# Optimization experiments

Hardware: AMD Instinct MI355X
Metric: run time of the kernel (lower is better)

## Reference

```python
import jax, jax.numpy as jnp
import numpy as np

B, S, HID, H, D, F = 8, 256, 1024, 16, 64, 64
BASE_LR = 0.1
MAX_STEPS = 4
EPS = 1e-5


def _ln(x, g, b):
    mu = jnp.mean(x, axis=-1, keepdims=True)
    var = jnp.var(x, axis=-1, keepdims=True)
    return (x - mu) * jax.lax.rsqrt(var + EPS) * g + b


def setup_inputs() -> dict:
    key = jax.random.key(0)
    ks = jax.random.split(key, 10)
    n = lambda i, shape, s=0.02: jax.random.normal(ks[i], shape, jnp.float32) * s
    return {
        "x": jax.random.normal(ks[0], (B, S, HID), jnp.float32),
        "wq": n(1, (HID, HID)),
        "wk": n(2, (HID, HID)),
        "wv": n(3, (HID, HID)),
        "fw_w1": n(4, (H, D, F), 0.05),
        "fw_b1": jnp.zeros((H, F), jnp.float32),
        "fw_w2": n(5, (H, F, D), 0.05),
        "fw_b2": jnp.zeros((H, D), jnp.float32),
        "fw_ln_g": jnp.ones((H, D), jnp.float32),
        "fw_ln_b": jnp.zeros((H, D), jnp.float32),
        "loss_w": n(6, (D, D)),
        "loss_b": jnp.zeros((D,), jnp.float32),
        "ttt_g": jnp.ones((H, D), jnp.float32),
        "ttt_b": jnp.zeros((H, D), jnp.float32),
        "wo": n(7, (HID, HID)),
        "wg": n(8, (HID, HID)),
        "pn_g": jnp.ones((HID,), jnp.float32),
        "pn_b": jnp.zeros((HID,), jnp.float32),
    }


def _fw_apply(p, kx):
    # per-head fast-weight MLP: kx (B,H,D) -> (B,H,D)
    w1, b1, w2, b2, lg, lb = p
    h = jax.nn.gelu(jnp.einsum('bhd,hdf->bhf', kx, w1) + b1)
    o = jnp.einsum('bhf,hfd->bhd', h, w2) + b2
    return _ln(o, lg, lb)


def _forward(x, wq, wk, wv, fw_w1, fw_b1, fw_w2, fw_b2, fw_ln_g, fw_ln_b,
             loss_w, loss_b, ttt_g, ttt_b, wo, wg, pn_g, pn_b):
    # projections (torch Linear with W stored as (in,out) here: y = x @ W)
    q = (x @ wq).reshape(B, S, H, D)
    k = (x @ wk).reshape(B, S, H, D)
    v = (x @ wv).reshape(B, S, H, D)
    # scan over tokens: xs shaped (S, B, H, D)
    qs = jnp.swapaxes(q, 0, 1)
    ks_ = jnp.swapaxes(k, 0, 1)
    vs = jnp.swapaxes(v, 0, 1)

    def token_step(p, qkv):
        q_t, k_t, v_t = qkv  # (B,H,D) each
        target = v_t - k_t

        def loss_fn(pp):
            z = _fw_apply(pp, k_t)
            pred = jnp.einsum('bhd,de->bhe', z, loss_w) + loss_b
            return jnp.mean((pred - target) ** 2)

        for _ in range(MAX_STEPS):
            g = jax.grad(loss_fn)(p)
            p = jax.tree.map(lambda a, gg: a - BASE_LR * gg, p, g)
        z = _fw_apply(p, k_t)
        z = _ln(z, ttt_g, ttt_b)  # per-head post-TTT LayerNorm
        return p, q_t + z

    p0 = (fw_w1, fw_b1, fw_w2, fw_b2, fw_ln_g, fw_ln_b)
    _, outs = jax.lax.scan(token_step, p0, (qs, ks_, vs))
    out = jnp.swapaxes(outs, 0, 1).reshape(B, S, HID)
    gated = jax.nn.gelu(x @ wg) * _ln(out, pn_g, pn_b)
    return gated @ wo


def reference(x, wq, wk, wv, fw_w1, fw_b1, fw_w2, fw_b2, fw_ln_g, fw_ln_b,
              loss_w, loss_b, ttt_g, ttt_b, wo, wg, pn_g, pn_b):
    return _forward(x, wq, wk, wv, fw_w1, fw_b1, fw_w2, fw_b2, fw_ln_g, fw_ln_b,
                    loss_w, loss_b, ttt_g, ttt_b, wo, wg, pn_g, pn_b)
```

## Files before the change

### kernel.cpp

```cpp
#include <hip/hip_runtime.h>

#define Bv 8
#define Sv 256
#define Hv 16
#define Dv 64
#define LR 0.1f
#define SCALE (2.0f / 8192.0f)

using bf16x8 = __attribute__((ext_vector_type(8))) short;
using bf16x4 = __attribute__((ext_vector_type(4))) short;
using f32x4  = __attribute__((ext_vector_type(4))) float;
using u32x4  = __attribute__((ext_vector_type(4))) unsigned;
#define MFMA16(A, B, C) __builtin_amdgcn_mfma_f32_16x16x32_bf16(A, B, C, 0, 0, 0)

constexpr int U_W1T = 0;
constexpr int U_W2T = 8704;
constexpr int U_W2R = 17408;
constexpr int U_G   = 26112;
constexpr int U_LwR = 34816;
constexpr int U_K   = 43520;
constexpr int U_H   = 45696;
constexpr int U_Z   = 47872;
constexpr int U_TG  = 50048;
constexpr int U_DO  = 52224;
constexpr int U_KT  = 54400;
constexpr int U_HT  = 55424;
constexpr int U_DOT = 56448;
constexpr int U_DAT = 57472;
constexpr int F_BASE = 29248;
constexpr int F_O   = F_BASE;
constexpr int F_XH  = F_BASE + 544;
constexpr int F_GD  = F_XH + 544;
constexpr int F_TGL = F_GD + 544;
constexpr int F_B1  = F_TGL + 544;
constexpr int F_B2  = F_B1 + 64;
constexpr int F_LG  = F_B2 + 64;
constexpr int F_LB  = F_LG + 64;
constexpr int F_C1  = F_LB + 64;
constexpr int F_TGm = F_C1 + 64;
constexpr int F_TBm = F_TGm + 64;
constexpr int F_RSTD = F_TBm + 64;
constexpr int U_KG  = (F_RSTD + 8) * 2;
constexpr int U_HT2 = U_KG + 256;
constexpr int LDS_BYTES = (U_HT2 + 1024) * 2;

__device__ __forceinline__ short bf_rn(float v) {
    unsigned u = __float_as_uint(v);
    unsigned r = u + 0x7fffu + ((u >> 16) & 1u);
    return (short)(r >> 16);
}
__device__ __forceinline__ void cvt1(float v, short &hi, short &lo) {
    hi = bf_rn(v);
    float hf = __uint_as_float(((unsigned)(unsigned short)hi) << 16);
    lo = bf_rn(v - hf);
}
__device__ __forceinline__ float bf2f(short u) {
    return __uint_as_float(((unsigned)(unsigned short)u) << 16);
}
__device__ __forceinline__ unsigned cvtpk(float a, float b) {
    unsigned r;
    asm("v_cvt_pk_bf16_f32 %0, %1, %2" : "=v"(r) : "v"(a), "v"(b));
    return r;
}
__device__ __forceinline__ void cvt2(float a, float b, unsigned &hw,
                                     unsigned &lw) {
    hw = cvtpk(a, b);
    float ra = a - __uint_as_float(hw << 16);
    float rb = b - __uint_as_float(hw & 0xffff0000u);
    lw = cvtpk(ra, rb);
}
template <int CTRL>
__device__ __forceinline__ float dpp_add(float v) {
    int s = __builtin_amdgcn_update_dpp(0, __float_as_int(v), CTRL, 0xF, 0xF,
                                        true);
    return v + __int_as_float(s);
}
__device__ __forceinline__ float red32(float v) {
    v = dpp_add<0xB1>(v);
    v = dpp_add<0x4E>(v);
    v = dpp_add<0x124>(v);
    v = dpp_add<0x128>(v);
    v += __shfl_xor(v, 16);
    return v;
}
__device__ __forceinline__ float fast_tanh(float u) {
    u = fminf(fmaxf(u, -10.f), 10.f);
    float e = __expf(2.0f * u);
    return (e - 1.0f) / (e + 1.0f);
}
__device__ __forceinline__ void gelu_both(float x, float &g, float &dg) {
    const float C0 = 0.7978845608028654f, A0 = 0.044715f;
    float x2 = x * x;
    float u = C0 * x * (1.0f + A0 * x2);
    float t = fast_tanh(u);
    g = 0.5f * x * (1.0f + t);
    float du = C0 * (1.0f + 3.0f * A0 * x2);
    dg = 0.5f * (1.0f + t) + 0.5f * x * (1.0f - t * t) * du;
}
__device__ __forceinline__ float gelu_f(float x) {
    const float C0 = 0.7978845608028654f, A0 = 0.044715f;
    float u = C0 * x * (1.0f + A0 * x * x);
    return 0.5f * x * (1.0f + fast_tanh(u));
}

__device__ __forceinline__ f32x4 mm64(const unsigned short *Ap,
                                      const unsigned short *Bp,
                                      int w, int c, int q) {
    const unsigned short *ar = Ap + c * 136 + 8 * q;
    const unsigned short *br = Bp + (16 * w + c) * 136 + 8 * q;
    bf16x8 ah0 = *(const bf16x8 *)(ar);
    bf16x8 al0 = *(const bf16x8 *)(ar + 64);
    bf16x8 bh0 = *(const bf16x8 *)(br);
    bf16x8 bl0 = *(const bf16x8 *)(br + 64);
    bf16x8 ah1 = *(const bf16x8 *)(ar + 32);
    bf16x8 al1 = *(const bf16x8 *)(ar + 96);
    bf16x8 bh1 = *(const bf16x8 *)(br + 32);
    bf16x8 bl1 = *(const bf16x8 *)(br + 96);
    f32x4 x0 = {0.f, 0.f, 0.f, 0.f}, x1 = {0.f, 0.f, 0.f, 0.f};
    x0 = MFMA16(ah0, bh0, x0); x1 = MFMA16(ah1, bh1, x1);
    x0 = MFMA16(al0, bh0, x0); x1 = MFMA16(al1, bh1, x1);
    x0 = MFMA16(ah0, bl0, x0); x1 = MFMA16(ah1, bl1, x1);
    return x0 + x1;
}

__device__ __forceinline__ void updW3(const bf16x8 *a4, bf16x8 b,
                                      float (&m)[16], unsigned short *WT,
                                      int w, int c, int q) {
    f32x4 g[4];
#pragma unroll
    for (int mt = 0; mt < 4; ++mt) {
        f32x4 z = {0.f, 0.f, 0.f, 0.f};
        g[mt] = MFMA16(a4[mt], b, z);
    }
    unsigned short *p0 = &WT[(16 * w + c) * 136 + 4 * q];
#pragma unroll
    for (int mt = 0; mt < 4; ++mt) {
        m[mt * 4 + 0] -= LR * g[mt][0];
        m[mt * 4 + 1] -= LR * g[mt][1];
        m[mt * 4 + 2] -= LR * g[mt][2];
        m[mt * 4 + 3] -= LR * g[mt][3];
        unsigned nh0, nl0, nh1, nl1;
        cvt2(m[mt * 4 + 0], m[mt * 4 + 1], nh0, nl0);
        cvt2(m[mt * 4 + 2], m[mt * 4 + 3], nh1, nl1);
        uint2 nh, nl;
        nh.x = nh0; nh.y = nh1;
        nl.x = nl0; nl.y = nl1;
        *(uint2 *)(p0 + 16 * mt) = nh;
        *(uint2 *)(p0 + 16 * mt + 64) = nl;
    }
}

__global__ __launch_bounds__(256) void ttt_scan(
    const float *__restrict__ q_g, const float *__restrict__ k_g,
    const float *__restrict__ v_g, float *__restrict__ out_g,
    const float *__restrict__ fw_w1, const float *__restrict__ fw_b1,
    const float *__restrict__ fw_w2, const float *__restrict__ fw_b2,
    const float *__restrict__ fw_lng, const float *__restrict__ fw_lnb,
    const float *__restrict__ loss_w, const float *__restrict__ loss_bv,
    const float *__restrict__ ttt_gv, const float *__restrict__ ttt_bv) {
    extern __shared__ char smem[];
    unsigned short *us = (unsigned short *)smem;
    float *fs = (float *)smem;

    unsigned short *W1T = us + U_W1T, *W2T = us + U_W2T, *W2R = us + U_W2R;
    unsigned short *Gp = us + U_G, *LwR = us + U_LwR;
    unsigned short *Kp = us + U_K, *Hp = us + U_H, *Zp = us + U_Z;
    unsigned short *TGp = us + U_TG, *DOp = us + U_DO;
    unsigned short *KT = us + U_KT, *HT0 = us + U_HT;
    unsigned short *DOT = us + U_DOT;
    unsigned short *KgT = us + U_KG, *HT1 = us + U_HT2;
    float *o_s = fs + F_O, *xh_s = fs + F_XH;
    float *b2_s = fs + F_B2, *lg_s = fs + F_LG;
    float *lb_s = fs + F_LB, *c1_s = fs + F_C1;
    float *tG_s = fs + F_TGm, *tB_s = fs + F_TBm, *rstd_s = fs + F_RSTD;

    const int h = blockIdx.x, tid = threadIdx.x;
    const int w = tid >> 6, lane = tid & 63, c = lane & 15, q = lane >> 4;
    const int bb = tid >> 5, j0 = (tid & 31) * 2;

    for (int i = tid; i < 4096; i += 256) {
        int r = i >> 6, cc = i & 63;
        short hi, lo;
        cvt1(fw_w1[h * 4096 + i], hi, lo);
        W1T[cc * 136 + r] = (unsigned short)hi;
        W1T[cc * 136 + 64 + r] = (unsigned short)lo;
        cvt1(fw_w2[h * 4096 + i], hi, lo);
        W2T[cc * 136 + r] = (unsigned short)hi;
        W2T[cc * 136 + 64 + r] = (unsigned short)lo;
        W2R[r * 136 + cc] = (unsigned short)hi;
        W2R[r * 136 + 64 + cc] = (unsigned short)lo;
        cvt1(loss_w[i], hi, lo);
        LwR[r * 136 + cc] = (unsigned short)hi;
        LwR[r * 136 + 64 + cc] = (unsigned short)lo;
    }
    for (int i = tid; i < 5 * 8 * 128; i += 256) {
        int a = i / 128, u = i % 128;
        int arr = a >> 3, row = 8 + (a & 7);
        unsigned short *base = (arr == 0) ? Kp : (arr == 1) ? Hp
                              : (arr == 2) ? Zp : (arr == 3) ? TGp : DOp;
        base[row * 136 + u] = 0;
    }
    float w1m[16], w2m[16], w2rm[16];
#pragma unroll
    for (int mt = 0; mt < 4; ++mt) {
#pragma unroll
        for (int r = 0; r < 4; ++r) {
            int el = 16 * mt + 4 * q + r;
            int row = 16 * w + c;
            w1m[mt * 4 + r] = fw_w1[h * 4096 + el * 64 + row];
            w2m[mt * 4 + r] = fw_w2[h * 4096 + el * 64 + row];
            w2rm[mt * 4 + r] = fw_w2[h * 4096 + row * 64 + el];
        }
    }
    __syncthreads();
#pragma unroll 1
    for (int mt = 0; mt < 4; ++mt) {
        f32x4 g = mm64(LwR + 16 * 136 * mt, LwR, w, c, q);
#pragma unroll
        for (int r = 0; r < 4; ++r) {
            short hi, lo;
            cvt1(g[r], hi, lo);
            int dr = 16 * mt + 4 * q + r, dc = 16 * w + c;
            Gp[dr * 136 + dc] = (unsigned short)hi;
            Gp[dr * 136 + 64 + dc] = (unsigned short)lo;
        }
    }
    if (tid < 64) {
        b2_s[tid] = fw_b2[h * 64 + tid];
        lg_s[tid] = fw_lng[h * 64 + tid];
        lb_s[tid] = fw_lnb[h * 64 + tid];
        tG_s[tid] = ttt_gv[h * 64 + tid];
        tB_s[tid] = ttt_bv[h * 64 + tid];
        float c1 = 0.f;
        for (int e = 0; e < 64; ++e) c1 += loss_bv[e] * loss_w[tid * 64 + e];
        c1_s[tid] = c1;
    }

    float2 pk, pv, pq, q_cur;
    {
        int idx = ((bb * Sv + 0) * Hv + h) * Dv + j0;
        float2 k0 = *(const float2 *)&k_g[idx];
        float2 v0 = *(const float2 *)&v_g[idx];
        q_cur = *(const float2 *)&q_g[idx];
        unsigned khw, klw;
        cvt2(k0.x, k0.y, khw, klw);
        *(unsigned *)&Kp[bb * 136 + j0] = khw;
        *(unsigned *)&Kp[bb * 136 + 64 + j0] = klw;
        KT[j0 * 16 + bb] = (unsigned short)khw;
        KT[j0 * 16 + 8 + bb] = (unsigned short)klw;
        KT[(j0 + 1) * 16 + bb] = (unsigned short)(khw >> 16);
        KT[(j0 + 1) * 16 + 8 + bb] = (unsigned short)(klw >> 16);
        unsigned thw, tlw;
        cvt2(v0.x - k0.x, v0.y - k0.y, thw, tlw);
        *(unsigned *)&TGp[bb * 136 + j0] = thw;
        *(unsigned *)&TGp[bb * 136 + 64 + j0] = tlw;
    }
    float b1_r = (q < 2) ? fw_b1[h * 64 + 16 * w + c] : 0.f;
    __syncthreads();
    float c1_r = c1_s[16 * w + c];
    f32x4 gd_r = {0.f, 0.f, 0.f, 0.f};
    f32x4 tgl_r = {0.f, 0.f, 0.f, 0.f};

#pragma unroll 1
    for (int t = 0; t < Sv; ++t) {
        if (t + 1 < Sv) {
            int idx2 = ((bb * Sv + t + 1) * Hv + h) * Dv + j0;
            pk = *(const float2 *)&k_g[idx2];
            pv = *(const float2 *)&v_g[idx2];
            pq = *(const float2 *)&q_g[idx2];
        }

        f32x4 acc1 = mm64(Kp, W1T, w, c, q);
        {
            f32x4 a2 = mm64(TGp, LwR, w, c, q);
            if (q < 2) {
#pragma unroll
                for (int r = 0; r < 4; ++r) tgl_r[r] = a2[r] - c1_r;
            }
        }
        if (w == 0) {
            f32x4 kg = mm64(Kp, Kp, 0, c, q);
            if (q < 2) {
#pragma unroll
                for (int r = 0; r < 4; ++r) {
                    short hi, lo;
                    cvt1(-LR * kg[r], hi, lo);
                    KgT[c * 16 + 4 * q + r] = (unsigned short)hi;
                    KgT[c * 16 + 8 + 4 * q + r] = (unsigned short)lo;
                }
            }
        }
        if (q < 2) {
            int col = 16 * w + c;
            float gv[4];
#pragma unroll
            for (int r = 0; r < 4; ++r) {
                float g, dg;
                gelu_both(acc1[r] + b1_r, g, dg);
                gv[r] = g;
                gd_r[r] = dg;
            }
            unsigned h01, l01, h23, l23;
            cvt2(gv[0], gv[1], h01, l01);
            cvt2(gv[2], gv[3], h23, l23);
            Hp[(4 * q + 0) * 136 + col] = (unsigned short)h01;
            Hp[(4 * q + 1) * 136 + col] = (unsigned short)(h01 >> 16);
            Hp[(4 * q + 2) * 136 + col] = (unsigned short)h23;
            Hp[(4 * q + 3) * 136 + col] = (unsigned short)(h23 >> 16);
            Hp[(4 * q + 0) * 136 + 64 + col] = (unsigned short)l01;
            Hp[(4 * q + 1) * 136 + 64 + col] = (unsigned short)(l01 >> 16);
            Hp[(4 * q + 2) * 136 + 64 + col] = (unsigned short)l23;
            Hp[(4 * q + 3) * 136 + 64 + col] = (unsigned short)(l23 >> 16);
            uint2 hh, hl;
            hh.x = h01; hh.y = h23;
            hl.x = l01; hl.y = l23;
            *(uint2 *)&HT0[col * 16 + 4 * q] = hh;
            *(uint2 *)&HT0[col * 16 + 8 + 4 * q] = hl;
        }
        __syncthreads();

#pragma unroll 1
        for (int step = 0; step < 4; ++step) {
            const unsigned short *HTr = (step & 1) ? HT1 : HT0;
            unsigned short *HTw = (step & 1) ? HT0 : HT1;
            f32x4 acc = mm64(Hp, W2T, w, c, q);
            if (q < 2) {
                float bias = b2_s[16 * w + c];
#pragma unroll
                for (int r = 0; r < 4; ++r)
                    o_s[(4 * q + r) * 68 + 16 * w + c] = acc[r] + bias;
            }
            __syncthreads();
            float xh0_r, xh1_r;
            {
                float2 xv = *(const float2 *)&o_s[bb * 68 + j0];
                float s = red32(xv.x + xv.y);
                float s2 = red32(xv.x * xv.x + xv.y * xv.y);
                float mu = s * (1.f / 64.f);
                float var = s2 * (1.f / 64.f) - mu * mu;
                float rs = rsqrtf(var + 1e-5f);
                float xh0 = (xv.x - mu) * rs, xh1 = (xv.y - mu) * rs;
                float2 xw; xw.x = xh0; xw.y = xh1;
                *(float2 *)&xh_s[bb * 68 + j0] = xw;
                float z0 = xh0 * lg_s[j0] + lb_s[j0];
                float z1 = xh1 * lg_s[j0 + 1] + lb_s[j0 + 1];
                unsigned zh, zl;
                cvt2(z0, z1, zh, zl);
                *(unsigned *)&Zp[bb * 136 + j0] = zh;
                *(unsigned *)&Zp[bb * 136 + 64 + j0] = zl;
                if ((tid & 31) == 0) rstd_s[bb] = rs;
                xh0_r = xh0; xh1_r = xh1;
            }
            __syncthreads();
            acc = mm64(Zp, Gp, w, c, q);
            if (q < 2) {
                int col = 16 * w + c;
#pragma unroll
                for (int r = 0; r < 4; ++r)
                    o_s[(4 * q + r) * 68 + col] = (acc[r] - tgl_r[r]) * SCALE;
            }
            __syncthreads();
            {
                float2 dzv = *(const float2 *)&o_s[bb * 68 + j0];
                float dxh0 = dzv.x * lg_s[j0], dxh1 = dzv.y * lg_s[j0 + 1];
                float S1 = red32(dxh0 + dxh1) * (1.f / 64.f);
                float S2 = red32(dxh0 * xh0_r + dxh1 * xh1_r) * (1.f / 64.f);
                float rs = rstd_s[bb];
                float do0 = rs * (dxh0 - S1 - xh0_r * S2);
                float do1 = rs * (dxh1 - S1 - xh1_r * S2);
                unsigned dh, dl;
                cvt2(do0, do1, dh, dl);
                *(unsigned *)&DOp[bb * 136 + j0] = dh;
                *(unsigned *)&DOp[bb * 136 + 64 + j0] = dl;
                DOT[j0 * 16 + bb] = (unsigned short)dh;
                DOT[j0 * 16 + 8 + bb] = (unsigned short)dl;
                DOT[(j0 + 1) * 16 + bb] = (unsigned short)(dh >> 16);
                DOT[(j0 + 1) * 16 + 8 + bb] = (unsigned short)(dl >> 16);
            }
            __syncthreads();
            bf16x8 zf8;
#pragma unroll
            for (int j = 0; j < 8; ++j) zf8[j] = 0;
            bf16x8 aK[4], aH[4], aD[4];
#pragma unroll
            for (int mt = 0; mt < 4; ++mt) {
                aK[mt] = *(const bf16x8 *)&KT[(16 * mt + c) * 16 + (q & 1) * 8];
                aH[mt] = *(const bf16x8 *)&HTr[(16 * mt + c) * 16 + (q & 1) * 8];
                aD[mt] = *(const bf16x8 *)&DOT[(16 * mt + c) * 16 + (q & 1) * 8];
            }
            bf16x8 bDO = zf8, bHT = zf8;
            if (q < 2) {
                bDO = *(const bf16x8 *)&DOT[(16 * w + c) * 16];
                bHT = *(const bf16x8 *)&HTr[(16 * w + c) * 16];
            } else if (q == 2) {
                bDO = *(const bf16x8 *)&DOT[(16 * w + c) * 16 + 8];
                bHT = *(const bf16x8 *)&HTr[(16 * w + c) * 16 + 8];
            }
            bf16x8 aKg = *(const bf16x8 *)&KgT[c * 16 + (q & 1) * 8];
            acc = mm64(DOp, W2R, w, c, q);
            {
                float b1sum = 0.f;
                uint2 th; th.x = 0u; th.y = 0u;
                uint2 tl; tl.x = 0u; tl.y = 0u;
                if (q < 2) {
                    float da0 = acc[0] * gd_r[0];
                    float da1 = acc[1] * gd_r[1];
                    float da2 = acc[2] * gd_r[2];
                    float da3 = acc[3] * gd_r[3];
                    b1sum = da0 + da1 + da2 + da3;
                    unsigned h01, l01, h23, l23;
                    cvt2(da0, da1, h01, l01);
                    cvt2(da2, da3, h23, l23);
                    th.x = h01; th.y = h23;
                    tl.x = l01; tl.y = l23;
                }
                b1sum += __shfl_xor(b1sum, 16);
                unsigned hx0 = (unsigned)__shfl((int)th.x, c);
                unsigned hy0 = (unsigned)__shfl((int)th.y, c);
                unsigned hx1 = (unsigned)__shfl((int)th.x, c + 16);
                unsigned hy1 = (unsigned)__shfl((int)th.y, c + 16);
                unsigned lx0 = (unsigned)__shfl((int)tl.x, c);
                unsigned ly0 = (unsigned)__shfl((int)tl.y, c);
                unsigned lx1 = (unsigned)__shfl((int)tl.x, c + 16);
                unsigned ly1 = (unsigned)__shfl((int)tl.y, c + 16);
                u32x4 Bw = {0u, 0u, 0u, 0u};
                if (q < 2) {
                    Bw[0] = hx0; Bw[1] = hy0; Bw[2] = hx1; Bw[3] = hy1;
                } else if (q == 2) {
                    Bw[0] = lx0; Bw[1] = ly0; Bw[2] = lx1; Bw[3] = ly1;
                }
                bf16x8 bDA = __builtin_bit_cast(bf16x8, Bw);
                updW3(aK, bDA, w1m, W1T, w, c, q);
                updW3(aH, bDO, w2m, W2T, w, c, q);
                updW3(aD, bHT, w2rm, W2R, w, c, q);
                if (w == 2) {
                    bf16x8 oh_ = *(const bf16x8 *)&DOT[lane * 16];
                    bf16x8 ol_ = *(const bf16x8 *)&DOT[lane * 16 + 8];
                    float db2 = 0.f;
#pragma unroll
                    for (int j = 0; j < 8; ++j)
                        db2 += bf2f(oh_[j]) + bf2f(ol_[j]);
                    b2_s[lane] -= LR * db2;
                } else if (w == 3) {
                    float dlb = 0.f, dlg = 0.f;
#pragma unroll
                    for (int b = 0; b < 8; ++b) {
                        float dzv = o_s[b * 68 + lane];
                        dlb += dzv;
                        dlg += dzv * xh_s[b * 68 + lane];
                    }
                    lb_s[lane] -= LR * dlb;
                    lg_s[lane] -= LR * dlg;
                }
                acc1 = MFMA16(aKg, bDA, acc1);
                b1_r -= LR * b1sum;
                if (q < 2) {
                    int col = 16 * w + c;
                    if (step < 3) {
                        float gv[4];
#pragma unroll
                        for (int r = 0; r < 4; ++r) {
                            float g, dg;
                            gelu_both(acc1[r] + b1_r, g, dg);
                            gv[r] = g;
                            gd_r[r] = dg;
                        }
                        unsigned h01, l01, h23, l23;
                        cvt2(gv[0], gv[1], h01, l01);
                        cvt2(gv[2], gv[3], h23, l23);
                        Hp[(4 * q + 0) * 136 + col] = (unsigned short)h01;
                        Hp[(4 * q + 1) * 136 + col] = (unsigned short)(h01 >> 16);
                        Hp[(4 * q + 2) * 136 + col] = (unsigned short)h23;
                        Hp[(4 * q + 3) * 136 + col] = (unsigned short)(h23 >> 16);
                        Hp[(4 * q + 0) * 136 + 64 + col] = (unsigned short)l01;
                        Hp[(4 * q + 1) * 136 + 64 + col] = (unsigned short)(l01 >> 16);
                        Hp[(4 * q + 2) * 136 + 64 + col] = (unsigned short)l23;
                        Hp[(4 * q + 3) * 136 + 64 + col] = (unsigned short)(l23 >> 16);
                        uint2 hh, hl;
                        hh.x = h01; hh.y = h23;
                        hl.x = l01; hl.y = l23;
                        *(uint2 *)&HTw[col * 16 + 4 * q] = hh;
                        *(uint2 *)&HTw[col * 16 + 8 + 4 * q] = hl;
                    } else {
                        float gv[4];
#pragma unroll
                        for (int r = 0; r < 4; ++r)
                            gv[r] = gelu_f(acc1[r] + b1_r);
                        unsigned h01, l01, h23, l23;
                        cvt2(gv[0], gv[1], h01, l01);
                        cvt2(gv[2], gv[3], h23, l23);
                        Hp[(4 * q + 0) * 136 + col] = (unsigned short)h01;
                        Hp[(4 * q + 1) * 136 + col] = (unsigned short)(h01 >> 16);
                        Hp[(4 * q + 2) * 136 + col] = (unsigned short)h23;
                        Hp[(4 * q + 3) * 136 + col] = (unsigned short)(h23 >> 16);
                        Hp[(4 * q + 0) * 136 + 64 + col] = (unsigned short)l01;
                        Hp[(4 * q + 1) * 136 + 64 + col] = (unsigned short)(l01 >> 16);
                        Hp[(4 * q + 2) * 136 + 64 + col] = (unsigned short)l23;
                        Hp[(4 * q + 3) * 136 + 64 + col] = (unsigned short)(l23 >> 16);
                    }
                }
            }
            __syncthreads();
        }

        f32x4 acc = mm64(Hp, W2T, w, c, q);
        if (q < 2) {
            float bias = b2_s[16 * w + c];
#pragma unroll
            for (int r = 0; r < 4; ++r)
                o_s[(4 * q + r) * 68 + 16 * w + c] = acc[r] + bias;
        }
        if (t + 1 < Sv) {
            unsigned khw, klw;
            cvt2(pk.x, pk.y, khw, klw);
            *(unsigned *)&Kp[bb * 136 + j0] = khw;
            *(unsigned *)&Kp[bb * 136 + 64 + j0] = klw;
            KT[j0 * 16 + bb] = (unsigned short)khw;
            KT[j0 * 16 + 8 + bb] = (unsigned short)klw;
            KT[(j0 + 1) * 16 + bb] = (unsigned short)(khw >> 16);
            KT[(j0 + 1) * 16 + 8 + bb] = (unsigned short)(klw >> 16);
            unsigned thw, tlw;
            cvt2(pv.x - pk.x, pv.y - pk.y, thw, tlw);
            *(unsigned *)&TGp[bb * 136 + j0] = thw;
            *(unsigned *)&TGp[bb * 136 + 64 + j0] = tlw;
        }
        __syncthreads();
        {
            float2 xv = *(const float2 *)&o_s[bb * 68 + j0];
            float s = red32(xv.x + xv.y);
            float s2 = red32(xv.x * xv.x + xv.y * xv.y);
            float mu = s * (1.f / 64.f);
            float var = s2 * (1.f / 64.f) - mu * mu;
            float rs = rsqrtf(var + 1e-5f);
            float z0 = (xv.x - mu) * rs * lg_s[j0] + lb_s[j0];
            float z1 = (xv.y - mu) * rs * lg_s[j0 + 1] + lb_s[j0 + 1];
            float sb = red32(z0 + z1);
            float s2b = red32(z0 * z0 + z1 * z1);
            float mu2 = sb * (1.f / 64.f);
            float var2 = s2b * (1.f / 64.f) - mu2 * mu2;
            float rs2 = rsqrtf(var2 + 1e-5f);
            float z20 = (z0 - mu2) * rs2 * tG_s[j0] + tB_s[j0];
            float z21 = (z1 - mu2) * rs2 * tG_s[j0 + 1] + tB_s[j0 + 1];
            int idx = ((bb * Sv + t) * Hv + h) * Dv + j0;
            float2 ov;
            ov.x = q_cur.x + z20;
            ov.y = q_cur.y + z21;
            *(float2 *)&out_g[idx] = ov;
            q_cur = pq;
        }
    }
}

__device__ __forceinline__ void gemm_body(
    const float *__restrict__ A, const float *__restrict__ B,
    float *__restrict__ C, const float *__restrict__ gate_ln,
    int N, int K, int mode, int bm, int bn,
    unsigned short *As, unsigned short *Bs, int tid) {
    const int w = tid >> 6, lane = tid & 63, c = lane & 15, q = lane >> 4;

    f32x4 acc[4] = {{0.f, 0.f, 0.f, 0.f}, {0.f, 0.f, 0.f, 0.f},
                    {0.f, 0.f, 0.f, 0.f}, {0.f, 0.f, 0.f, 0.f}};
    const int srow = tid >> 2, sseg = (tid & 3) * 16;
    const int nB = tid & 63, kb = (tid >> 6) * 16;

    for (int k0 = 0; k0 < K; k0 += 64) {
        {
            const float *src = A + (long)(bm + srow) * K + k0 + sseg;
#pragma unroll
            for (int j = 0; j < 16; j += 2) {
                float2 v = *(const float2 *)(src + j);
                unsigned hw, lw;
                cvt2(v.x, v.y, hw, lw);
                *(unsigned *)&As[srow * 136 + sseg + j] = hw;
                *(unsigned *)&As[srow * 136 + 64 + sseg + j] = lw;
            }
        }
        {
            const float *bsrc = B + (long)(k0 + kb) * N + bn + nB;
#pragma unroll
            for (int j = 0; j < 16; j += 2) {
                float f0 = bsrc[(long)j * N];
                float f1 = bsrc[(long)(j + 1) * N];
                unsigned hw, lw;
                cvt2(f0, f1, hw, lw);
                *(unsigned *)&Bs[nB * 136 + kb + j] = hw;
                *(unsigned *)&Bs[nB * 136 + 64 + kb + j] = lw;
            }
        }
        __syncthreads();
#pragma unroll
        for (int kc = 0; kc < 2; ++kc) {
            const unsigned short *br =
                &Bs[(16 * w + c) * 136 + kc * 32 + 8 * q];
            bf16x8 bh = *(const bf16x8 *)(br);
            bf16x8 bl = *(const bf16x8 *)(br + 64);
#pragma unroll
            for (int mt = 0; mt < 4; ++mt) {
                const unsigned short *ar =
                    &As[(16 * mt + c) * 136 + kc * 32 + 8 * q];
                bf16x8 ah = *(const bf16x8 *)(ar);
                bf16x8 al = *(const bf16x8 *)(ar + 64);
                acc[mt] = MFMA16(ah, bh, acc[mt]);
                acc[mt] = MFMA16(al, bh, acc[mt]);
                acc[mt] = MFMA16(ah, bl, acc[mt]);
            }
        }
        __syncthreads();
    }
#pragma unroll
    for (int mt = 0; mt < 4; ++mt) {
#pragma unroll
        for (int r = 0; r < 4; ++r) {
            int row = bm + 16 * mt + 4 * q + r;
            int col = bn + 16 * w + c;
            float val = acc[mt][r];
            if (mode == 1)
                val = gelu_f(val) * gate_ln[(long)row * N + col];
            C[(long)row * N + col] = val;
        }
    }
}

__global__ __launch_bounds__(256) void gemm_bf16(
    const float *__restrict__ A, const float *__restrict__ B,
    float *__restrict__ C, const float *__restrict__ gate_ln,
    int M, int N, int K, int mode) {
    __shared__ unsigned short As[64 * 136];
    __shared__ unsigned short Bs[64 * 136];
    gemm_body(A, B, C, gate_ln, N, K, mode, blockIdx.y * 64, blockIdx.x * 64,
              As, Bs, threadIdx.x);
}

__global__ __launch_bounds__(256) void gemm_qkv(
    const float *__restrict__ A, const float *__restrict__ Wq_,
    const float *__restrict__ Wk_, const float *__restrict__ Wv_,
    float *__restrict__ Cq, float *__restrict__ Ck, float *__restrict__ Cv_,
    int N, int K) {
    __shared__ unsigned short As[64 * 136];
    __shared__ unsigned short Bs[64 * 136];
    const int mat = blockIdx.x >> 4;
    const int bn = (blockIdx.x & 15) * 64;
    const float *Bmat = (mat == 0) ? Wq_ : (mat == 1) ? Wk_ : Wv_;
    float *Cmat = (mat == 0) ? Cq : (mat == 1) ? Ck : Cv_;
    gemm_body(A, Bmat, Cmat, nullptr, N, K, 0, blockIdx.y * 64, bn, As, Bs,
              threadIdx.x);
}

__global__ __launch_bounds__(256) void row_ln(const float *__restrict__ in,
                                              float *__restrict__ out,
                                              const float *__restrict__ g,
                                              const float *__restrict__ b) {
    __shared__ float sred[4], s2red[4];
    const int row = blockIdx.x;
    const int tid = threadIdx.x;
    const float *x = in + (long)row * 1024;
    float4 v = *(const float4 *)(x + tid * 4);
    float s = v.x + v.y + v.z + v.w;
    float s2 = v.x * v.x + v.y * v.y + v.z * v.z + v.w * v.w;
#pragma unroll
    for (int m = 1; m <= 32; m <<= 1) {
        s += __shfl_xor(s, m);
        s2 += __shfl_xor(s2, m);
    }
    if ((tid & 63) == 0) {
        sred[tid >> 6] = s;
        s2red[tid >> 6] = s2;
    }
    __syncthreads();
    float S = sred[0] + sred[1] + sred[2] + sred[3];
    float S2 = s2red[0] + s2red[1] + s2red[2] + s2red[3];
    float mu = S * (1.f / 1024.f);
    float var = S2 * (1.f / 1024.f) - mu * mu;
    float rs = rsqrtf(var + 1e-5f);
    float o[4] = {v.x, v.y, v.z, v.w};
    float4 ov;
    float r[4];
#pragma unroll
    for (int i = 0; i < 4; ++i) {
        int col = tid * 4 + i;
        r[i] = (o[i] - mu) * rs * g[col] + b[col];
    }
    ov.x = r[0]; ov.y = r[1]; ov.z = r[2]; ov.w = r[3];
    *(float4 *)(out + (long)row * 1024 + tid * 4) = ov;
}

extern "C" void kernel_launch(void *const *d_in, const int *in_sizes, int n_in,
                              void *d_out, int out_size, void *d_ws,
                              size_t ws_size, hipStream_t stream) {
    const float *x = (const float *)d_in[0];
    const float *wq = (const float *)d_in[1];
    const float *wk = (const float *)d_in[2];
    const float *wv = (const float *)d_in[3];
    const float *fw_w1 = (const float *)d_in[4];
    const float *fw_b1 = (const float *)d_in[5];
    const float *fw_w2 = (const float *)d_in[6];
    const float *fw_b2 = (const float *)d_in[7];
    const float *fw_lng = (const float *)d_in[8];
    const float *fw_lnb = (const float *)d_in[9];
    const float *loss_w = (const float *)d_in[10];
    const float *loss_b = (const float *)d_in[11];
    const float *ttt_g = (const float *)d_in[12];
    const float *ttt_b = (const float *)d_in[13];
    const float *wo = (const float *)d_in[14];
    const float *wg = (const float *)d_in[15];
    const float *pn_g = (const float *)d_in[16];
    const float *pn_b = (const float *)d_in[17];

    const long MAT = 2048L * 1024L;
    float *q_ws = (float *)d_ws;
    float *k_ws = q_ws + MAT;
    float *v_ws = k_ws + MAT;
    float *out_ws = v_ws + MAT;
    float *ln_ws = k_ws;
    float *gated_ws = v_ws;

    dim3 gq(16 * 3, 2048 / 64), gg(1024 / 64, 2048 / 64), bt(256);
    hipLaunchKernelGGL(gemm_qkv, gq, bt, 0, stream, x, wq, wk, wv,
                       q_ws, k_ws, v_ws, 1024, 1024);

    (void)hipFuncSetAttribute((const void *)ttt_scan,
                              hipFuncAttributeMaxDynamicSharedMemorySize,
                              LDS_BYTES);
    hipLaunchKernelGGL(ttt_scan, dim3(16), dim3(256), LDS_BYTES, stream,
                       q_ws, k_ws, v_ws, out_ws, fw_w1, fw_b1, fw_w2, fw_b2,
                       fw_lng, fw_lnb, loss_w, loss_b, ttt_g, ttt_b);

    hipLaunchKernelGGL(row_ln, dim3(2048), dim3(256), 0, stream, out_ws, ln_ws,
                       pn_g, pn_b);
    hipLaunchKernelGGL(gemm_bf16, gg, bt, 0, stream, x, wg, gated_ws, ln_ws,
                       2048, 1024, 1024, 1);
    hipLaunchKernelGGL(gemm_bf16, gg, bt, 0, stream, gated_ws, wo,
                       (float *)d_out, (const float *)nullptr, 2048, 1024,
                       1024, 0);
}
```

Before: 3.702 ms.

## Overlap gate GEMM with the TTT scan by running it in extra blocks

The x@wg gate GEMM with its GELU now runs in 512 extra blocks of the ttt_scan launch, so it executes on otherwise idle CUs while the 16 scan blocks work. Its result is written to the output buffer as scratch. A small elementwise kernel then multiplies it by the layer-normed TTT output, replacing the fused gate GEMM that used to run after the scan. The cost is an extra read and write of a 2048x1024 tensor, plus the extra blocks taking the large dynamic LDS allocation, which can limit how many fit per CU.

Result: no change. 3.700 ms (-0.0%).

```diff
diff --git a/kernel.cpp b/kernel.cpp
--- a/kernel.cpp
+++ b/kernel.cpp
@@ -150,6 +150,78 @@
     }
 }
 
+__device__ __forceinline__ void gemm_body(
+    const float *__restrict__ A, const float *__restrict__ B,
+    float *__restrict__ C, const float *__restrict__ gate_ln,
+    int N, int K, int mode, int bm, int bn,
+    unsigned short *As, unsigned short *Bs, int tid) {
+    const int w = tid >> 6, lane = tid & 63, c = lane & 15, q = lane >> 4;
+
+    f32x4 acc[4] = {{0.f, 0.f, 0.f, 0.f}, {0.f, 0.f, 0.f, 0.f},
+                    {0.f, 0.f, 0.f, 0.f}, {0.f, 0.f, 0.f, 0.f}};
+    const int srow = tid >> 2, sseg = (tid & 3) * 16;
+    const int nB = tid & 63, kb = (tid >> 6) * 16;
+
+    for (int k0 = 0; k0 < K; k0 += 64) {
+        {
+            const float *src = A + (long)(bm + srow) * K + k0 + sseg;
+#pragma unroll
+            for (int j = 0; j < 16; j += 2) {
+                float2 v = *(const float2 *)(src + j);
+                unsigned hw, lw;
+                cvt2(v.x, v.y, hw, lw);
+                *(unsigned *)&As[srow * 136 + sseg + j] = hw;
+                *(unsigned *)&As[srow * 136 + 64 + sseg + j] = lw;
+            }
+        }
+        {
+            const float *bsrc = B + (long)(k0 + kb) * N + bn + nB;
+#pragma unroll
+            for (int j = 0; j < 16; j += 2) {
+                float f0 = bsrc[(long)j * N];
+                float f1 = bsrc[(long)(j + 1) * N];
+                unsigned hw, lw;
+                cvt2(f0, f1, hw, lw);
+                *(unsigned *)&Bs[nB * 136 + kb + j] = hw;
+                *(unsigned *)&Bs[nB * 136 + 64 + kb + j] = lw;
+            }
+        }
+        __syncthreads();
+#pragma unroll
+        for (int kc = 0; kc < 2; ++kc) {
+            const unsigned short *br =
+                &Bs[(16 * w + c) * 136 + kc * 32 + 8 * q];
+            bf16x8 bh = *(const bf16x8 *)(br);
+            bf16x8 bl = *(const bf16x8 *)(br + 64);
+#pragma unroll
+            for (int mt = 0; mt < 4; ++mt) {
+                const unsigned short *ar =
+                    &As[(16 * mt + c) * 136 + kc * 32 + 8 * q];
+                bf16x8 ah = *(const bf16x8 *)(ar);
+                bf16x8 al = *(const bf16x8 *)(ar + 64);
+                acc[mt] = MFMA16(ah, bh, acc[mt]);
+                acc[mt] = MFMA16(al, bh, acc[mt]);
+                acc[mt] = MFMA16(ah, bl, acc[mt]);
+            }
+        }
+        __syncthreads();
+    }
+#pragma unroll
+    for (int mt = 0; mt < 4; ++mt) {
+#pragma unroll
+        for (int r = 0; r < 4; ++r) {
+            int row = bm + 16 * mt + 4 * q + r;
+            int col = bn + 16 * w + c;
+            float val = acc[mt][r];
+            if (mode == 1)
+                val = gelu_f(val) * gate_ln[(long)row * N + col];
+            else if (mode == 3)
+                val = gelu_f(val);
+            C[(long)row * N + col] = val;
+        }
+    }
+}
+
 __global__ __launch_bounds__(256) void ttt_scan(
     const float *__restrict__ q_g, const float *__restrict__ k_g,
     const float *__restrict__ v_g, float *__restrict__ out_g,
@@ -157,10 +229,20 @@
     const float *__restrict__ fw_w2, const float *__restrict__ fw_b2,
     const float *__restrict__ fw_lng, const float *__restrict__ fw_lnb,
     const float *__restrict__ loss_w, const float *__restrict__ loss_bv,
-    const float *__restrict__ ttt_gv, const float *__restrict__ ttt_bv) {
+    const float *__restrict__ ttt_gv, const float *__restrict__ ttt_bv,
+    const float *__restrict__ gx, const float *__restrict__ gwg,
+    float *__restrict__ ggo) {
     extern __shared__ char smem[];
     unsigned short *us = (unsigned short *)smem;
     float *fs = (float *)smem;
+    const int tid = threadIdx.x;
+
+    if (blockIdx.x >= Hv) {
+        int bid = blockIdx.x - Hv;
+        gemm_body(gx, gwg, ggo, nullptr, 1024, 1024, 3,
+                  (bid >> 4) * 64, (bid & 15) * 64, us, us + 64 * 136, tid);
+        return;
+    }
 
     unsigned short *W1T = us + U_W1T, *W2T = us + U_W2T, *W2R = us + U_W2R;
     unsigned short *Gp = us + U_G, *LwR = us + U_LwR;
@@ -174,7 +256,7 @@
     float *lb_s = fs + F_LB, *c1_s = fs + F_C1;
     float *tG_s = fs + F_TGm, *tB_s = fs + F_TBm, *rstd_s = fs + F_RSTD;
 
-    const int h = blockIdx.x, tid = threadIdx.x;
+    const int h = blockIdx.x;
     const int w = tid >> 6, lane = tid & 63, c = lane & 15, q = lane >> 4;
     const int bb = tid >> 5, j0 = (tid & 31) * 2;
 
@@ -551,76 +633,6 @@
     }
 }
 
-__device__ __forceinline__ void gemm_body(
-    const float *__restrict__ A, const float *__restrict__ B,
-    float *__restrict__ C, const float *__restrict__ gate_ln,
-    int N, int K, int mode, int bm, int bn,
-    unsigned short *As, unsigned short *Bs, int tid) {
-    const int w = tid >> 6, lane = tid & 63, c = lane & 15, q = lane >> 4;
-
-    f32x4 acc[4] = {{0.f, 0.f, 0.f, 0.f}, {0.f, 0.f, 0.f, 0.f},
-                    {0.f, 0.f, 0.f, 0.f}, {0.f, 0.f, 0.f, 0.f}};
-    const int srow = tid >> 2, sseg = (tid & 3) * 16;
-    const int nB = tid & 63, kb = (tid >> 6) * 16;
-
-    for (int k0 = 0; k0 < K; k0 += 64) {
-        {
-            const float *src = A + (long)(bm + srow) * K + k0 + sseg;
-#pragma unroll
-            for (int j = 0; j < 16; j += 2) {
-                float2 v = *(const float2 *)(src + j);
-                unsigned hw, lw;
-                cvt2(v.x, v.y, hw, lw);
-                *(unsigned *)&As[srow * 136 + sseg + j] = hw;
-                *(unsigned *)&As[srow * 136 + 64 + sseg + j] = lw;
-            }
-        }
-        {
-            const float *bsrc = B + (long)(k0 + kb) * N + bn + nB;
-#pragma unroll
-            for (int j = 0; j < 16; j += 2) {
-                float f0 = bsrc[(long)j * N];
-                float f1 = bsrc[(long)(j + 1) * N];
-                unsigned hw, lw;
-                cvt2(f0, f1, hw, lw);
-                *(unsigned *)&Bs[nB * 136 + kb + j] = hw;
-                *(unsigned *)&Bs[nB * 136 + 64 + kb + j] = lw;
-            }
-        }
-        __syncthreads();
-#pragma unroll
-        for (int kc = 0; kc < 2; ++kc) {
-            const unsigned short *br =
-                &Bs[(16 * w + c) * 136 + kc * 32 + 8 * q];
-            bf16x8 bh = *(const bf16x8 *)(br);
-            bf16x8 bl = *(const bf16x8 *)(br + 64);
-#pragma unroll
-            for (int mt = 0; mt < 4; ++mt) {
-                const unsigned short *ar =
-                    &As[(16 * mt + c) * 136 + kc * 32 + 8 * q];
-                bf16x8 ah = *(const bf16x8 *)(ar);
-                bf16x8 al = *(const bf16x8 *)(ar + 64);
-                acc[mt] = MFMA16(ah, bh, acc[mt]);
-                acc[mt] = MFMA16(al, bh, acc[mt]);
-                acc[mt] = MFMA16(ah, bl, acc[mt]);
-            }
-        }
-        __syncthreads();
-    }
-#pragma unroll
-    for (int mt = 0; mt < 4; ++mt) {
-#pragma unroll
-        for (int r = 0; r < 4; ++r) {
-            int row = bm + 16 * mt + 4 * q + r;
-            int col = bn + 16 * w + c;
-            float val = acc[mt][r];
-            if (mode == 1)
-                val = gelu_f(val) * gate_ln[(long)row * N + col];
-            C[(long)row * N + col] = val;
-        }
-    }
-}
-
 __global__ __launch_bounds__(256) void gemm_bf16(
     const float *__restrict__ A, const float *__restrict__ B,
     float *__restrict__ C, const float *__restrict__ gate_ln,
@@ -644,6 +656,20 @@
     float *Cmat = (mat == 0) ? Cq : (mat == 1) ? Ck : Cv_;
     gemm_body(A, Bmat, Cmat, nullptr, N, K, 0, blockIdx.y * 64, bn, As, Bs,
               threadIdx.x);
+}
+
+__global__ __launch_bounds__(256) void mul_gate(
+    const float *__restrict__ a, const float *__restrict__ g2,
+    float *__restrict__ o2) {
+    long i = ((long)blockIdx.x * 256 + threadIdx.x) * 4;
+    float4 va = *(const float4 *)&a[i];
+    float4 vb = *(const float4 *)&g2[i];
+    float4 vo;
+    vo.x = va.x * vb.x;
+    vo.y = va.y * vb.y;
+    vo.z = va.z * vb.z;
+    vo.w = va.w * vb.w;
+    *(float4 *)&o2[i] = vo;
 }
 
 __global__ __launch_bounds__(256) void row_ln(const float *__restrict__ in,
@@ -713,6 +739,7 @@
     float *out_ws = v_ws + MAT;
     float *ln_ws = k_ws;
     float *gated_ws = v_ws;
+    float *ggr = (float *)d_out;
 
     dim3 gq(16 * 3, 2048 / 64), gg(1024 / 64, 2048 / 64), bt(256);
     hipLaunchKernelGGL(gemm_qkv, gq, bt, 0, stream, x, wq, wk, wv,
@@ -721,14 +748,15 @@
     (void)hipFuncSetAttribute((const void *)ttt_scan,
                               hipFuncAttributeMaxDynamicSharedMemorySize,
                               LDS_BYTES);
-    hipLaunchKernelGGL(ttt_scan, dim3(16), dim3(256), LDS_BYTES, stream,
+    hipLaunchKernelGGL(ttt_scan, dim3(16 + 512), dim3(256), LDS_BYTES, stream,
                        q_ws, k_ws, v_ws, out_ws, fw_w1, fw_b1, fw_w2, fw_b2,
-                       fw_lng, fw_lnb, loss_w, loss_b, ttt_g, ttt_b);
+                       fw_lng, fw_lnb, loss_w, loss_b, ttt_g, ttt_b,
+                       x, wg, ggr);
 
     hipLaunchKernelGGL(row_ln, dim3(2048), dim3(256), 0, stream, out_ws, ln_ws,
                        pn_g, pn_b);
-    hipLaunchKernelGGL(gemm_bf16, gg, bt, 0, stream, x, wg, gated_ws, ln_ws,
-                       2048, 1024, 1024, 1);
+    hipLaunchKernelGGL(mul_gate, dim3(2048), bt, 0, stream,
+                       (const float *)ggr, ln_ws, gated_ws);
     hipLaunchKernelGGL(gemm_bf16, gg, bt, 0, stream, gated_ws, wo,
                        (float *)d_out, (const float *)nullptr, 2048, 1024,
                        1024, 0);
```
